# Optimization experiments

Hardware: AMD Instinct MI355X
Metric: run time of the kernel (lower is better)

Reference implementation:

```python
import jax, jax.numpy as jnp
import numpy as np
from jax import lax

B, C, H, W = 8, 64, 64, 64
C8 = C // 8
EPS = 1e-5


def setup_inputs() -> dict:
    key = jax.random.key(0)
    ks = jax.random.split(key, 10)
    s = lambda *sh: 0.02
    inp = {
        "x": jax.random.normal(ks[0], (B, C, H, W), dtype=jnp.float32),
        "conv_b_w": jax.random.normal(ks[1], (C8, C), dtype=jnp.float32) * 0.05,
        "conv_b_b": jnp.zeros((C8,), jnp.float32),
        "conv_c_w": jax.random.normal(ks[2], (C8, C), dtype=jnp.float32) * 0.05,
        "conv_c_b": jnp.zeros((C8,), jnp.float32),
        "conv_d_w": jax.random.normal(ks[3], (C, C), dtype=jnp.float32) * 0.05,
        "conv_d_b": jnp.zeros((C,), jnp.float32),
        "alpha": jnp.zeros((1,), jnp.float32) + 0.1,  # learned PAM scale
        "beta": jnp.zeros((1,), jnp.float32) + 0.1,   # learned CAM scale
        "conv_w": jax.random.normal(ks[4], (2 * C, C, 3, 3), dtype=jnp.float32) * 0.02,
        "conv_bias": jnp.zeros((2 * C,), jnp.float32),
        "bn_gamma": jnp.ones((2 * C,), jnp.float32),
        "bn_beta": jnp.zeros((2 * C,), jnp.float32),
    }
    return inp


def _conv1x1(x, w, b):
    # x: [B,C,H,W], w: [O,C] -> [B,O,H,W]
    return jnp.einsum('oc,bchw->bohw', w, x) + b[None, :, None, None]


def _forward(x, conv_b_w, conv_b_b, conv_c_w, conv_c_b, conv_d_w, conv_d_b,
             alpha, beta, conv_w, conv_bias, bn_gamma, bn_beta):
    b, c, h, w = x.shape
    n = h * w
    # ---- Position Attention Module ----
    feat_b = _conv1x1(x, conv_b_w, conv_b_b).reshape(b, C8, n)   # [B,C8,N]
    feat_c = _conv1x1(x, conv_c_w, conv_c_b).reshape(b, C8, n)   # [B,C8,N]
    # torch: bmm(feat_b^T [B,N,C8], feat_c [B,C8,N]) -> [B,N,N]
    attn_s = jax.nn.softmax(jnp.einsum('bcn,bcm->bnm', feat_b, feat_c), axis=-1)
    feat_d = _conv1x1(x, conv_d_w, conv_d_b).reshape(b, c, n)    # [B,C,N]
    # torch: bmm(feat_d, attn_s^T) -> out[b,c,n] = sum_m feat_d[b,c,m]*attn[b,n,m]
    feat_e = jnp.einsum('bcm,bnm->bcn', feat_d, attn_s).reshape(b, c, h, w)
    x = alpha[0] * feat_e + x
    # ---- Channel Attention Module ----
    fa = x.reshape(b, c, n)                                      # [B,C,N]
    att = jnp.einsum('bcn,bdn->bcd', fa, fa)                     # [B,C,C]
    att_new = jnp.max(att, axis=-1, keepdims=True) - att
    att = jax.nn.softmax(att_new, axis=-1)
    fe = jnp.einsum('bcd,bdn->bcn', att, fa).reshape(b, c, h, w)
    x = beta[0] * fe + x
    # ---- conv3x3 + BN (batch stats) + ReLU + maxpool(2,2,pad=(1,0)) ----
    out = lax.conv_general_dilated(x, conv_w, (1, 1), ((1, 1), (1, 1)),
                                   dimension_numbers=('NCHW', 'OIHW', 'NCHW'))
    out = out + conv_bias[None, :, None, None]
    mean = jnp.mean(out, axis=(0, 2, 3), keepdims=True)
    var = jnp.var(out, axis=(0, 2, 3), keepdims=True)
    out = (out - mean) * lax.rsqrt(var + EPS)
    out = out * bn_gamma[None, :, None, None] + bn_beta[None, :, None, None]
    out = jax.nn.relu(out)
    # MaxPool2d(kernel=2, stride=2, padding=(1,0)): -inf padding on height only
    out = lax.reduce_window(out, -jnp.inf, lax.max,
                            (1, 1, 2, 2), (1, 1, 2, 2),
                            ((0, 0), (0, 0), (1, 1), (0, 0)))
    return out


def reference(x, conv_b_w, conv_b_b, conv_c_w, conv_c_b, conv_d_w, conv_d_b,
              alpha, beta, conv_w, conv_bias, bn_gamma, bn_beta):
    return _forward(x, conv_b_w, conv_b_b, conv_c_w, conv_c_b, conv_d_w, conv_d_b,
                    alpha, beta, conv_w, conv_bias, bn_gamma, bn_beta)
```

## Files before the change

kernel.cpp:

```cpp
#include <hip/hip_runtime.h>

using f32x4  = __attribute__((ext_vector_type(4))) float;
using bf16x8 = __attribute__((ext_vector_type(8))) short;
using u32x4  = __attribute__((ext_vector_type(4))) unsigned int;
using u32x2  = __attribute__((ext_vector_type(2))) unsigned int;
typedef unsigned short u16;

__device__ __forceinline__ u16 f2bf(float f) {
  unsigned u = __float_as_uint(f);
  unsigned r = (u + 0x7FFFu + ((u >> 16) & 1u)) >> 16;
  return (u16)r;
}

#if __has_builtin(__builtin_amdgcn_exp2f)
#define FAST_EXP2(x) __builtin_amdgcn_exp2f(x)
#else
#define FAST_EXP2(x) __expf(0.6931471805599453f * (x))
#endif

#define LOG2E 1.4426950408889634f

__global__ void __launch_bounds__(256) k1_conv1x1(
    const float* __restrict__ x, const float* __restrict__ wB, const float* __restrict__ bB,
    const float* __restrict__ wC, const float* __restrict__ bC,
    const float* __restrict__ wD, const float* __restrict__ bD,
    u16* __restrict__ featBb, u16* __restrict__ featCb, u16* __restrict__ featD,
    const float* __restrict__ cw, u16* __restrict__ wb) {
  const int t = threadIdx.x;
  const int b = blockIdx.y;
  const int z = blockIdx.z;
  if (z == 3) {
    int gid = (b * 16 + blockIdx.x) * 256 + t;
#pragma unroll
    for (int k = 0; k < 3; ++k) {
      int F = gid + k * 32768;
      if (F < 73728) {
        int j = F & 7, lane = (F >> 3) & 63, T = F >> 9;
        int tap = T >> 4, g = (T >> 1) & 7, kc = T & 1;
        int l16 = lane & 15, quad = lane >> 4;
        int oc = g * 16 + l16, ic = kc * 32 + quad * 8 + j;
        wb[F] = f2bf(cw[(oc * 64 + ic) * 9 + tap]);
      }
    }
    return;
  }
  __shared__ float W[2048];
  __shared__ float Bias[32];
  const int n = blockIdx.x * 256 + t;
  if (z == 0) {
    for (int i = t; i < 512; i += 256) W[i] = wB[i];
    for (int i = t; i < 512; i += 256) W[512 + i] = wC[i];
    if (t < 8) Bias[t] = bB[t];
    if (t >= 8 && t < 16) Bias[t] = bC[t - 8];
  } else {
    const float* wsrc = wD + (z - 1) * 2048;
    for (int i = t; i < 2048; i += 256) W[i] = wsrc[i];
    if (t < 32) Bias[t] = bD[(z - 1) * 32 + t];
  }
  __syncthreads();
  float xv[64];
#pragma unroll
  for (int c = 0; c < 64; ++c) xv[c] = x[((b * 64 + c) << 12) + n];
  if (z == 0) {
    float o[16];
#pragma unroll
    for (int k = 0; k < 16; ++k) {
      f32x4 s = {0.f, 0.f, 0.f, 0.f};
#pragma unroll
      for (int cq = 0; cq < 16; ++cq) {
        f32x4 wv = *(const f32x4*)&W[k * 64 + cq * 4];
        f32x4 xq = {xv[cq * 4], xv[cq * 4 + 1], xv[cq * 4 + 2], xv[cq * 4 + 3]};
        s += wv * xq;
      }
      o[k] = Bias[k] + s[0] + s[1] + s[2] + s[3];
    }
    int base = ((b << 12) + n) * 8;
    u32x4 pb, pc;
#pragma unroll
    for (int i = 0; i < 4; ++i) {
      pb[i] = (unsigned)f2bf(o[2 * i] * LOG2E) | ((unsigned)f2bf(o[2 * i + 1] * LOG2E) << 16);
      pc[i] = (unsigned)f2bf(o[8 + 2 * i]) | ((unsigned)f2bf(o[8 + 2 * i + 1]) << 16);
    }
    *(u32x4*)&featBb[base] = pb;
    *(u32x4*)&featCb[base] = pc;
  } else {
#pragma unroll 4
    for (int k = 0; k < 32; ++k) {
      f32x4 s = {0.f, 0.f, 0.f, 0.f};
#pragma unroll
      for (int cq = 0; cq < 16; ++cq) {
        f32x4 wv = *(const f32x4*)&W[k * 64 + cq * 4];
        f32x4 xq = {xv[cq * 4], xv[cq * 4 + 1], xv[cq * 4 + 2], xv[cq * 4 + 3]};
        s += wv * xq;
      }
      float val = Bias[k] + s[0] + s[1] + s[2] + s[3];
      featD[((b * 64 + (z - 1) * 32 + k) << 12) + n] = f2bf(val);
    }
  }
}

__global__ void __launch_bounds__(256) k2_pam_part(
    const u16* __restrict__ fBb, const u16* __restrict__ fCb, const u16* __restrict__ fD,
    u16* __restrict__ numPart, float* __restrict__ denPart) {
  __shared__ u16 Kf[128 * 8];
  __shared__ u16 Df[64 * 132];
  __shared__ u16 Ps4[4][2][16 * 72];
  const int t = threadIdx.x, b = blockIdx.y, z = blockIdx.z;
  const int w = t >> 6, lane = t & 63, quad = lane >> 4, l16 = lane & 15;
  const int nb = blockIdx.x * 128 + w * 32;
  u16* myPs = &Ps4[w][0][0];

  bf16x8 bq[2];
#pragma unroll
  for (int j = 0; j < 2; ++j) {
    bq[j] = *(const bf16x8*)&fBb[(((b << 12) + nb + j * 16 + l16) << 3)];
    if (quad != 0) bq[j] = (bf16x8)(short)0;
  }

  f32x4 acc[4][2];
#pragma unroll
  for (int ct = 0; ct < 4; ++ct)
#pragma unroll
    for (int j = 0; j < 2; ++j) acc[ct][j] = (f32x4){0.f, 0.f, 0.f, 0.f};
  float denp[2] = {0.f, 0.f};
  const int mz = z << 10;

  for (int ch = 0; ch < 8; ++ch) {
    const int m0 = mz + (ch << 7);
    __syncthreads();
    if (t < 128) *(u32x4*)&Kf[t * 8] = *(const u32x4*)&fCb[(((b << 12) + m0 + t) << 3)];
#pragma unroll
    for (int h = 0; h < 4; ++h) {
      int idx = h * 256 + t;
      int r = idx >> 4, mo = (idx & 15) << 3;
      *(u32x4*)&Df[r * 132 + mo] = *(const u32x4*)&fD[((b * 64 + r) << 12) + m0 + mo];
    }
    __syncthreads();
#pragma unroll
    for (int sub = 0; sub < 2; ++sub) {
      const int ms = sub * 64;
#pragma unroll
      for (int mt = 0; mt < 4; ++mt) {
        bf16x8 af = *(const bf16x8*)&Kf[(ms + mt * 16 + l16) * 8];
#pragma unroll
        for (int jj = 0; jj < 2; ++jj) {
          f32x4 zero = {0.f, 0.f, 0.f, 0.f};
          f32x4 s = __builtin_amdgcn_mfma_f32_16x16x32_bf16(af, bq[jj], zero, 0, 0, 0);
          float e0 = FAST_EXP2(s[0]), e1 = FAST_EXP2(s[1]), e2 = FAST_EXP2(s[2]), e3 = FAST_EXP2(s[3]);
          denp[jj] += (e0 + e1) + (e2 + e3);
          u32x2 pk;
          pk[0] = __builtin_amdgcn_perm(__float_as_uint(e1), __float_as_uint(e0), 0x07060302u);
          pk[1] = __builtin_amdgcn_perm(__float_as_uint(e3), __float_as_uint(e2), 0x07060302u);
          *(u32x2*)&myPs[jj * 1152 + l16 * 72 + mt * 16 + quad * 4] = pk;
        }
      }
#pragma unroll
      for (int kc = 0; kc < 2; ++kc) {
        bf16x8 bv0 = *(const bf16x8*)&myPs[0 * 1152 + l16 * 72 + kc * 32 + quad * 8];
        bf16x8 bv1 = *(const bf16x8*)&myPs[1 * 1152 + l16 * 72 + kc * 32 + quad * 8];
#pragma unroll
        for (int ct = 0; ct < 4; ++ct) {
          bf16x8 av = *(const bf16x8*)&Df[(ct * 16 + l16) * 132 + ms + kc * 32 + quad * 8];
          acc[ct][0] = __builtin_amdgcn_mfma_f32_16x16x32_bf16(av, bv0, acc[ct][0], 0, 0, 0);
          acc[ct][1] = __builtin_amdgcn_mfma_f32_16x16x32_bf16(av, bv1, acc[ct][1], 0, 0, 0);
        }
      }
    }
  }
#pragma unroll
  for (int j = 0; j < 2; ++j) {
    denp[j] += __shfl_xor(denp[j], 16);
    denp[j] += __shfl_xor(denp[j], 32);
  }
  const int zb = z * 8 + b;
#pragma unroll
  for (int ct = 0; ct < 4; ++ct)
#pragma unroll
    for (int j = 0; j < 2; ++j)
#pragma unroll
      for (int r = 0; r < 4; ++r) {
        int c = ct * 16 + quad * 4 + r;
        numPart[((zb * 64 + c) << 12) + nb + j * 16 + l16] = (u16)(__float_as_uint(acc[ct][j][r]) >> 16);
      }
  if (quad == 0)
#pragma unroll
    for (int j = 0; j < 2; ++j) denPart[(zb << 12) + nb + j * 16 + l16] = denp[j];
}

__global__ void __launch_bounds__(256) k3_gram(
    const u16* __restrict__ numPart, const float* __restrict__ denPart,
    const float* __restrict__ x, const float* __restrict__ alpha,
    float* __restrict__ x1, float* __restrict__ attPart) {
  __shared__ float X[64 * 132];
  __shared__ float Dinv[128];
  const int t = threadIdx.x, b = blockIdx.y, cx = blockIdx.x;
  const int n0 = cx * 128;
  if (t < 128) {
    float den = 0.f;
#pragma unroll
    for (int z = 0; z < 4; ++z) den += denPart[(((z * 8 + b) << 12)) + n0 + t];
    Dinv[t] = alpha[0] / den;
  }
  __syncthreads();
  for (int idx = t; idx < 4096; idx += 256) {
    int row = idx >> 6, cp = (idx & 63) * 2;
    int gi = ((b * 64 + row) << 12) + n0 + cp;
    float num0 = 0.f, num1 = 0.f;
#pragma unroll
    for (int z = 0; z < 4; ++z) {
      unsigned v = *(const unsigned*)&numPart[(((z * 8 + b) * 64 + row) << 12) + n0 + cp];
      num0 += __uint_as_float(v << 16);
      num1 += __uint_as_float(v & 0xFFFF0000u);
    }
    float v0 = num0 * Dinv[cp] + x[gi];
    float v1 = num1 * Dinv[cp + 1] + x[gi + 1];
    X[row * 132 + cp] = v0;
    X[row * 132 + cp + 1] = v1;
    x1[gi] = v0;
    x1[gi + 1] = v1;
  }
  __syncthreads();
  const int cg = t >> 4, dg = t & 15;
  f32x4 acc[4][4];
#pragma unroll
  for (int i = 0; i < 4; ++i)
#pragma unroll
    for (int k = 0; k < 4; ++k) acc[i][k] = (f32x4){0.f, 0.f, 0.f, 0.f};
  for (int nq0 = 0; nq0 < 32; ++nq0) {
    int nq = (nq0 + dg) & 31;
    f32x4 a[4], bb[4];
#pragma unroll
    for (int i = 0; i < 4; ++i) a[i] = *(const f32x4*)&X[(cg * 4 + i) * 132 + nq * 4];
#pragma unroll
    for (int k = 0; k < 4; ++k) bb[k] = *(const f32x4*)&X[(dg * 4 + k) * 132 + nq * 4];
#pragma unroll
    for (int i = 0; i < 4; ++i)
#pragma unroll
      for (int k = 0; k < 4; ++k) acc[i][k] += a[i] * bb[k];
  }
#pragma unroll
  for (int i = 0; i < 4; ++i)
#pragma unroll
    for (int k = 0; k < 4; ++k) {
      f32x4 s = acc[i][k];
      attPart[((b * 32 + cx) * 64 + cg * 4 + i) * 64 + dg * 4 + k] = s[0] + s[1] + s[2] + s[3];
    }
}

__global__ void __launch_bounds__(256) k4_softmax(const float* __restrict__ attPart, float* __restrict__ attP) {
  const int b = blockIdx.y, t = threadIdx.x;
  const int c = (blockIdx.x << 2) + (t >> 6), d = t & 63;
  float v = 0.f;
  for (int p = 0; p < 32; ++p) v += attPart[((b * 32 + p) * 64 + c) * 64 + d];
  float mn = v;
#pragma unroll
  for (int off = 1; off < 64; off <<= 1) mn = fminf(mn, __shfl_xor(mn, off));
  float e = __expf(mn - v);
  float sum = e;
#pragma unroll
  for (int off = 1; off < 64; off <<= 1) sum += __shfl_xor(sum, off);
  attP[(b * 64 + c) * 64 + d] = e / sum;
}

__global__ void __launch_bounds__(256) k5_apply(
    const float* __restrict__ attP, const float* __restrict__ x1,
    const float* __restrict__ beta, u16* __restrict__ x2b) {
  __shared__ float A[64 * 68];
  const int t = threadIdx.x, b = blockIdx.y;
  for (int idx = t; idx < 4096; idx += 256) A[(idx >> 6) * 68 + (idx & 63)] = attP[(b << 12) + idx];
  __syncthreads();
  const int n = blockIdx.x * 256 + t;
  float xv[64];
#pragma unroll
  for (int d = 0; d < 64; ++d) xv[d] = x1[((b * 64 + d) << 12) + n];
  const float bv = beta[0];
  u16* orow = x2b + (((size_t)(b << 12) + n) << 6);
#pragma unroll 2
  for (int cg = 0; cg < 8; ++cg) {
    unsigned pk[4];
#pragma unroll
    for (int ci = 0; ci < 8; ++ci) {
      int c = cg * 8 + ci;
      f32x4 s = {0.f, 0.f, 0.f, 0.f};
#pragma unroll
      for (int dq = 0; dq < 16; ++dq) {
        f32x4 avv = *(const f32x4*)&A[c * 68 + dq * 4];
        f32x4 xq = {xv[dq * 4], xv[dq * 4 + 1], xv[dq * 4 + 2], xv[dq * 4 + 3]};
        s += avv * xq;
      }
      float fe = s[0] + s[1] + s[2] + s[3];
      float val = bv * fe + xv[c];
      unsigned h = f2bf(val);
      if ((ci & 1) == 0) pk[ci >> 1] = h;
      else pk[ci >> 1] |= h << 16;
    }
    *(u32x4*)&orow[cg * 8] = (u32x4){pk[0], pk[1], pk[2], pk[3]};
  }
}

__global__ void __launch_bounds__(256) k6_mfma(const u16* __restrict__ x2b, const u16* __restrict__ wb,
                                               float* __restrict__ y) {
  __shared__ u16 Xl[3 * 66 * 72];
  const int t = threadIdx.x, b = blockIdx.y, h = blockIdx.x;
  for (int idx = t; idx < 3 * 66 * 8; idx += 256) {
    int r = idx / 528;
    int rem = idx - r * 528;
    int c = rem >> 3, icq = rem & 7;
    int gy = h - 1 + r, gx = c - 1;
    u32x4 v = {0u, 0u, 0u, 0u};
    if (gy >= 0 && gy < 64 && gx >= 0 && gx < 64)
      v = *(const u32x4*)&x2b[(((size_t)(b << 6 | gy) << 6) + gx) * 64 + icq * 8];
    *(u32x4*)&Xl[(r * 66 + c) * 72 + icq * 8] = v;
  }
  __syncthreads();
  const int w = t >> 6, lane = t & 63, quad = lane >> 4, l16 = lane & 15;
  const int mBase = (w & 1) * 64;
  const int og = (w & 1) * 4;
  const int nBase = (w >> 1) * 32;
  f32x4 acc[4][2];
#pragma unroll
  for (int ot = 0; ot < 4; ++ot)
#pragma unroll
    for (int nt = 0; nt < 2; ++nt) acc[ot][nt] = (f32x4){0.f, 0.f, 0.f, 0.f};
#pragma unroll 3
  for (int tap = 0; tap < 9; ++tap) {
    const int dy = tap / 3, dx = tap - dy * 3;
    bf16x8 af[4][2];
#pragma unroll
    for (int ot = 0; ot < 4; ++ot)
#pragma unroll
      for (int kc = 0; kc < 2; ++kc)
        af[ot][kc] = *(const bf16x8*)&wb[((((tap * 8 + og + ot) * 2 + kc) << 6) + lane) << 3];
#pragma unroll
    for (int nt = 0; nt < 2; ++nt) {
      const int prow = dy * 66 + nBase + nt * 16 + l16 + dx;
#pragma unroll
      for (int kc = 0; kc < 2; ++kc) {
        bf16x8 bv = *(const bf16x8*)&Xl[prow * 72 + kc * 32 + quad * 8];
#pragma unroll
        for (int ot = 0; ot < 4; ++ot)
          acc[ot][nt] = __builtin_amdgcn_mfma_f32_16x16x32_bf16(af[ot][kc], bv, acc[ot][nt], 0, 0, 0);
      }
    }
  }
#pragma unroll
  for (int ot = 0; ot < 4; ++ot)
#pragma unroll
    for (int nt = 0; nt < 2; ++nt)
#pragma unroll
      for (int r = 0; r < 4; ++r) {
        int oc = mBase + ot * 16 + quad * 4 + r;
        int pix = nBase + nt * 16 + l16;
        y[((b * 128 + oc) << 12) + (h << 6) + pix] = acc[ot][nt][r];
      }
}

__global__ void __launch_bounds__(256) k7_part(const float* __restrict__ y, float* __restrict__ pstats) {
  const int ch = blockIdx.x, q = blockIdx.y, t = threadIdx.x;
  float s = 0.f, ss = 0.f;
#pragma unroll
  for (int bb = 0; bb < 2; ++bb) {
    const float* p = y + (((q * 2 + bb) * 128 + ch) << 12);
#pragma unroll
    for (int i = 0; i < 16; ++i) { float v = p[i * 256 + t]; s += v; ss += v * v; }
  }
#pragma unroll
  for (int off = 1; off < 64; off <<= 1) { s += __shfl_xor(s, off); ss += __shfl_xor(ss, off); }
  __shared__ float rs[4], rss[4];
  if ((t & 63) == 0) { rs[t >> 6] = s; rss[t >> 6] = ss; }
  __syncthreads();
  if (t == 0) {
    pstats[ch * 8 + q * 2]     = rs[0] + rs[1] + rs[2] + rs[3];
    pstats[ch * 8 + q * 2 + 1] = rss[0] + rss[1] + rss[2] + rss[3];
  }
}

__global__ void __launch_bounds__(256) k8_pool(const float* __restrict__ y, const float* __restrict__ pstats,
                                               const float* __restrict__ gamma, const float* __restrict__ bbeta,
                                               float* __restrict__ out) {
  const int bc = blockIdx.x;
  const int ch = bc & 127;
  float S = 0.f, SS = 0.f;
#pragma unroll
  for (int q = 0; q < 4; ++q) { S += pstats[ch * 8 + q * 2]; SS += pstats[ch * 8 + q * 2 + 1]; }
  const float mean = S * (1.f / 32768.f);
  const float var = SS * (1.f / 32768.f) - mean * mean;
  const float sc = gamma[ch] * rsqrtf(var + 1e-5f);
  const float sh = bbeta[ch] - mean * sc;
  const float* p = y + (bc << 12);
  float* op = out + bc * (33 * 32);
  for (int i = threadIdx.x; i < 33 * 32; i += 256) {
    int oh = i >> 5, ow = i & 31;
    int r0 = 2 * oh - 1, r1 = 2 * oh;
    float m = 0.f;
    if (r0 >= 0) {
      m = fmaxf(m, p[r0 * 64 + 2 * ow] * sc + sh);
      m = fmaxf(m, p[r0 * 64 + 2 * ow + 1] * sc + sh);
    }
    if (r1 <= 63) {
      m = fmaxf(m, p[r1 * 64 + 2 * ow] * sc + sh);
      m = fmaxf(m, p[r1 * 64 + 2 * ow + 1] * sc + sh);
    }
    op[i] = m;
  }
}

extern "C" void kernel_launch(void* const* d_in, const int* in_sizes, int n_in,
                              void* d_out, int out_size, void* d_ws, size_t ws_size,
                              hipStream_t stream) {
  const float* x      = (const float*)d_in[0];
  const float* wB     = (const float*)d_in[1];
  const float* bB     = (const float*)d_in[2];
  const float* wC     = (const float*)d_in[3];
  const float* bC     = (const float*)d_in[4];
  const float* wD     = (const float*)d_in[5];
  const float* bD     = (const float*)d_in[6];
  const float* alpha  = (const float*)d_in[7];
  const float* beta   = (const float*)d_in[8];
  const float* cw     = (const float*)d_in[9];
  const float* gamma  = (const float*)d_in[11];
  const float* bnbeta = (const float*)d_in[12];

  char* ws = (char*)d_ws;
  u16*   featBb  = (u16*)  (ws + 0);
  u16*   featCb  = (u16*)  (ws + 524288);
  u16*   fDb     = (u16*)  (ws + 1048576);
  u16*   x2b     = (u16*)  (ws + 0);
  float* x1      = (float*)(ws + 5242880);
  u16*   numPart = (u16*)  (ws + 13631488);
  float* y       = (float*)(ws + 13631488);
  float* denPart = (float*)(ws + 30408704);
  float* attPart = (float*)(ws + 30932992);
  float* attP    = (float*)(ws + 35127296);
  u16*   wb      = (u16*)  (ws + 35258368);
  float* pstats  = (float*)(ws + 35405824);
  float* outp    = (float*)d_out;

  k1_conv1x1<<<dim3(16, 8, 4), 256, 0, stream>>>(x, wB, bB, wC, bC, wD, bD, featBb, featCb, fDb, cw, wb);
  k2_pam_part<<<dim3(32, 8, 4), 256, 0, stream>>>(featBb, featCb, fDb, numPart, denPart);
  k3_gram<<<dim3(32, 8), 256, 0, stream>>>(numPart, denPart, x, alpha, x1, attPart);
  k4_softmax<<<dim3(16, 8), 256, 0, stream>>>(attPart, attP);
  k5_apply<<<dim3(16, 8), 256, 0, stream>>>(attP, x1, beta, x2b);
  k6_mfma<<<dim3(64, 8), 256, 0, stream>>>(x2b, wb, y);
  k7_part<<<dim3(128, 4), 256, 0, stream>>>(y, pstats);
  k8_pool<<<dim3(1024), 256, 0, stream>>>(y, pstats, gamma, bnbeta, outp);
}
```

Baseline: 220.0 us.

## Switch PAM attention to 32x32 MFMA with in-register P via permlane swap

Rewrites the position-attention kernel to use 32x32x16 bf16 MFMA tiles instead of 16x16x32. The exponentiated scores are now repacked in registers with v_permlane32_swap, so there is no LDS round-trip for P, and the key tile is read straight from global memory instead of LDS. Each wave now covers 64 query positions, which halves the grid. The cost is fewer blocks for occupancy, plus wasted MFMA work because the C8=8 reduction is zero-padded to 16.

Result: no change. 216.9 us (-1.4%).

```diff
diff --git a/kernel.cpp b/kernel.cpp
--- a/kernel.cpp
+++ b/kernel.cpp
@@ -1,6 +1,7 @@
 #include <hip/hip_runtime.h>
 
 using f32x4  = __attribute__((ext_vector_type(4))) float;
+using f32x16 = __attribute__((ext_vector_type(16))) float;
 using bf16x8 = __attribute__((ext_vector_type(8))) short;
 using u32x4  = __attribute__((ext_vector_type(4))) unsigned int;
 using u32x2  = __attribute__((ext_vector_type(2))) unsigned int;
@@ -19,6 +20,10 @@
 #endif
 
 #define LOG2E 1.4426950408889634f
+
+__device__ __forceinline__ void permswap32(unsigned& a, unsigned& b) {
+  asm volatile("v_permlane32_swap_b32 %0, %1" : "+v"(a), "+v"(b));
+}
 
 __global__ void __launch_bounds__(256) k1_conv1x1(
     const float* __restrict__ x, const float* __restrict__ wB, const float* __restrict__ bB,
@@ -102,89 +107,93 @@
 __global__ void __launch_bounds__(256) k2_pam_part(
     const u16* __restrict__ fBb, const u16* __restrict__ fCb, const u16* __restrict__ fD,
     u16* __restrict__ numPart, float* __restrict__ denPart) {
-  __shared__ u16 Kf[128 * 8];
   __shared__ u16 Df[64 * 132];
-  __shared__ u16 Ps4[4][2][16 * 72];
   const int t = threadIdx.x, b = blockIdx.y, z = blockIdx.z;
-  const int w = t >> 6, lane = t & 63, quad = lane >> 4, l16 = lane & 15;
-  const int nb = blockIdx.x * 128 + w * 32;
-  u16* myPs = &Ps4[w][0][0];
+  const int w = t >> 6, lane = t & 63, l32 = lane & 31, hi = lane >> 5;
+  const int nb = blockIdx.x * 256 + w * 64;
+  const int mz = z << 10;
 
   bf16x8 bq[2];
 #pragma unroll
   for (int j = 0; j < 2; ++j) {
-    bq[j] = *(const bf16x8*)&fBb[(((b << 12) + nb + j * 16 + l16) << 3)];
-    if (quad != 0) bq[j] = (bf16x8)(short)0;
-  }
-
-  f32x4 acc[4][2];
-#pragma unroll
-  for (int ct = 0; ct < 4; ++ct)
-#pragma unroll
-    for (int j = 0; j < 2; ++j) acc[ct][j] = (f32x4){0.f, 0.f, 0.f, 0.f};
+    bf16x8 v = (bf16x8)(short)0;
+    if (hi == 0) v = *(const bf16x8*)&fBb[(((b << 12) + nb + j * 32 + l32) << 3)];
+    bq[j] = v;
+  }
+
+  f32x16 acc[2][2];
+#pragma unroll
+  for (int ct = 0; ct < 2; ++ct)
+#pragma unroll
+    for (int j = 0; j < 2; ++j) acc[ct][j] = (f32x16)(0.0f);
   float denp[2] = {0.f, 0.f};
-  const int mz = z << 10;
 
   for (int ch = 0; ch < 8; ++ch) {
     const int m0 = mz + (ch << 7);
     __syncthreads();
-    if (t < 128) *(u32x4*)&Kf[t * 8] = *(const u32x4*)&fCb[(((b << 12) + m0 + t) << 3)];
-#pragma unroll
-    for (int h = 0; h < 4; ++h) {
-      int idx = h * 256 + t;
+#pragma unroll
+    for (int hh = 0; hh < 4; ++hh) {
+      int idx = hh * 256 + t;
       int r = idx >> 4, mo = (idx & 15) << 3;
       *(u32x4*)&Df[r * 132 + mo] = *(const u32x4*)&fD[((b * 64 + r) << 12) + m0 + mo];
     }
     __syncthreads();
 #pragma unroll
-    for (int sub = 0; sub < 2; ++sub) {
-      const int ms = sub * 64;
-#pragma unroll
-      for (int mt = 0; mt < 4; ++mt) {
-        bf16x8 af = *(const bf16x8*)&Kf[(ms + mt * 16 + l16) * 8];
-#pragma unroll
-        for (int jj = 0; jj < 2; ++jj) {
-          f32x4 zero = {0.f, 0.f, 0.f, 0.f};
-          f32x4 s = __builtin_amdgcn_mfma_f32_16x16x32_bf16(af, bq[jj], zero, 0, 0, 0);
-          float e0 = FAST_EXP2(s[0]), e1 = FAST_EXP2(s[1]), e2 = FAST_EXP2(s[2]), e3 = FAST_EXP2(s[3]);
-          denp[jj] += (e0 + e1) + (e2 + e3);
-          u32x2 pk;
-          pk[0] = __builtin_amdgcn_perm(__float_as_uint(e1), __float_as_uint(e0), 0x07060302u);
-          pk[1] = __builtin_amdgcn_perm(__float_as_uint(e3), __float_as_uint(e2), 0x07060302u);
-          *(u32x2*)&myPs[jj * 1152 + l16 * 72 + mt * 16 + quad * 4] = pk;
+    for (int mt2 = 0; mt2 < 4; ++mt2) {
+      bf16x8 af = (bf16x8)(short)0;
+      if (hi == 0) af = *(const bf16x8*)&fCb[(((b << 12) + m0 + mt2 * 32 + l32) << 3)];
+
+      unsigned u0[8], u1[8];
+#pragma unroll
+      for (int j = 0; j < 2; ++j) {
+        f32x16 s = __builtin_amdgcn_mfma_f32_32x32x16_bf16(af, bq[j], (f32x16)(0.0f), 0, 0, 0);
+        unsigned* uu = j ? u1 : u0;
+        float dsum = 0.f;
+#pragma unroll
+        for (int i = 0; i < 8; ++i) {
+          float e0 = FAST_EXP2(s[2 * i]);
+          float e1 = FAST_EXP2(s[2 * i + 1]);
+          dsum += e0 + e1;
+          uu[i] = __builtin_amdgcn_perm(__float_as_uint(e1), __float_as_uint(e0), 0x07060302u);
         }
-      }
+        denp[j] += dsum;
+      }
+      permswap32(u0[0], u0[2]); permswap32(u0[1], u0[3]);
+      permswap32(u0[4], u0[6]); permswap32(u0[5], u0[7]);
+      permswap32(u1[0], u1[2]); permswap32(u1[1], u1[3]);
+      permswap32(u1[4], u1[6]); permswap32(u1[5], u1[7]);
+
 #pragma unroll
       for (int kc = 0; kc < 2; ++kc) {
-        bf16x8 bv0 = *(const bf16x8*)&myPs[0 * 1152 + l16 * 72 + kc * 32 + quad * 8];
-        bf16x8 bv1 = *(const bf16x8*)&myPs[1 * 1152 + l16 * 72 + kc * 32 + quad * 8];
-#pragma unroll
-        for (int ct = 0; ct < 4; ++ct) {
-          bf16x8 av = *(const bf16x8*)&Df[(ct * 16 + l16) * 132 + ms + kc * 32 + quad * 8];
-          acc[ct][0] = __builtin_amdgcn_mfma_f32_16x16x32_bf16(av, bv0, acc[ct][0], 0, 0, 0);
-          acc[ct][1] = __builtin_amdgcn_mfma_f32_16x16x32_bf16(av, bv1, acc[ct][1], 0, 0, 0);
+        u32x4 q0 = {u0[4 * kc], u0[4 * kc + 1], u0[4 * kc + 2], u0[4 * kc + 3]};
+        u32x4 q1 = {u1[4 * kc], u1[4 * kc + 1], u1[4 * kc + 2], u1[4 * kc + 3]};
+        bf16x8 bv0 = *(bf16x8*)&q0;
+        bf16x8 bv1 = *(bf16x8*)&q1;
+#pragma unroll
+        for (int ct = 0; ct < 2; ++ct) {
+          bf16x8 av = *(const bf16x8*)&Df[(ct * 32 + l32) * 132 + mt2 * 32 + kc * 16 + hi * 8];
+          acc[ct][0] = __builtin_amdgcn_mfma_f32_32x32x16_bf16(av, bv0, acc[ct][0], 0, 0, 0);
+          acc[ct][1] = __builtin_amdgcn_mfma_f32_32x32x16_bf16(av, bv1, acc[ct][1], 0, 0, 0);
         }
       }
     }
   }
+
+  const int zb = z * 8 + b;
+#pragma unroll
+  for (int ct = 0; ct < 2; ++ct)
+#pragma unroll
+    for (int j = 0; j < 2; ++j)
+#pragma unroll
+      for (int r = 0; r < 16; ++r) {
+        int c = ct * 32 + (r & 3) + ((r >> 2) << 3) + (hi << 2);
+        numPart[((zb * 64 + c) << 12) + nb + j * 32 + l32] = (u16)(__float_as_uint(acc[ct][j][r]) >> 16);
+      }
 #pragma unroll
   for (int j = 0; j < 2; ++j) {
-    denp[j] += __shfl_xor(denp[j], 16);
-    denp[j] += __shfl_xor(denp[j], 32);
-  }
-  const int zb = z * 8 + b;
-#pragma unroll
-  for (int ct = 0; ct < 4; ++ct)
-#pragma unroll
-    for (int j = 0; j < 2; ++j)
-#pragma unroll
-      for (int r = 0; r < 4; ++r) {
-        int c = ct * 16 + quad * 4 + r;
-        numPart[((zb * 64 + c) << 12) + nb + j * 16 + l16] = (u16)(__float_as_uint(acc[ct][j][r]) >> 16);
-      }
-  if (quad == 0)
-#pragma unroll
-    for (int j = 0; j < 2; ++j) denPart[(zb << 12) + nb + j * 16 + l16] = denp[j];
+    float d = denp[j] + __shfl_xor(denp[j], 32);
+    if (hi == 0) denPart[(zb << 12) + nb + j * 32 + l32] = d;
+  }
 }
 
 __global__ void __launch_bounds__(256) k3_gram(
@@ -437,7 +446,7 @@
   float* outp    = (float*)d_out;
 
   k1_conv1x1<<<dim3(16, 8, 4), 256, 0, stream>>>(x, wB, bB, wC, bC, wD, bD, featBb, featCb, fDb, cw, wb);
-  k2_pam_part<<<dim3(32, 8, 4), 256, 0, stream>>>(featBb, featCb, fDb, numPart, denPart);
+  k2_pam_part<<<dim3(16, 8, 4), 256, 0, stream>>>(featBb, featCb, fDb, numPart, denPart);
   k3_gram<<<dim3(32, 8), 256, 0, stream>>>(numPart, denPart, x, alpha, x1, attPart);
   k4_softmax<<<dim3(16, 8), 256, 0, stream>>>(attPart, attP);
   k5_apply<<<dim3(16, 8), 256, 0, stream>>>(attP, x1, beta, x2b);
```
